# Performance work log

Hardware: AMD Instinct MI355X
Metric: run time of the kernel (lower is better)

## Reference

```python
import jax, jax.numpy as jnp
import numpy as np

B, S, D = 4, 2048, 1024
H, HD = 8, 128
EPS = 1e-5
NEG = -1e30


def layernorm(x, w, b):
    mu = jnp.mean(x, axis=-1, keepdims=True)
    var = jnp.mean(jnp.square(x - mu), axis=-1, keepdims=True)
    return (x - mu) * jax.lax.rsqrt(var + EPS) * w + b


def rmsnorm(x, w):
    ms = jnp.mean(jnp.square(x), axis=-1, keepdims=True)
    return x * jax.lax.rsqrt(ms + EPS) * w


def setup_inputs() -> dict:
    key = jax.random.key(0)
    ks = jax.random.split(key, 8)
    scale = 0.02
    return {
        "layer_input": jax.random.normal(ks[0], (B, S, D), jnp.float32),
        "positions": jnp.broadcast_to(jnp.arange(S, dtype=jnp.int32), (B, S)),
        "ln_in_w": jnp.ones((D,), jnp.float32),
        "ln_in_b": jnp.zeros((D,), jnp.float32),
        "W_uvqk": jax.random.normal(ks[1], (D, 4 * H * HD), jnp.float32) * scale,
        "b_uvqk": jax.random.normal(ks[2], (4 * H * HD,), jnp.float32) * scale,
        "ln_out_w": jnp.ones((H * HD,), jnp.float32),
        "ln_out_b": jnp.zeros((H * HD,), jnp.float32),
        "W_proj": jax.random.normal(ks[3], (H * HD, D), jnp.float32) * scale,
        "rms_w": jnp.ones((D,), jnp.float32),
        "W1": jax.random.normal(ks[4], (D, 2 * D), jnp.float32) * scale,
        "W2": jax.random.normal(ks[5], (D, D), jnp.float32) * scale,
    }


def reference(layer_input, positions, ln_in_w, ln_in_b, W_uvqk, b_uvqk,
              ln_out_w, ln_out_b, W_proj, rms_w, W1, W2):
    # --- HSTU attention block ---
    normed = layernorm(layer_input, ln_in_w, ln_in_b)              # [B,S,D]
    mixed = jax.nn.silu(normed @ W_uvqk + b_uvqk)                  # [B,S,4*H*HD]
    user, value, query, key = jnp.split(mixed, 4, axis=-1)
    q = query.reshape(B, S, H, HD)
    k = key.reshape(B, S, H, HD)
    v = value.reshape(B, S, H, HD)
    alpha = 1.0 / np.sqrt(HD).astype(np.float32)
    scores = jnp.einsum("bqhd,bkhd->bhqk", q, k) * alpha           # [B,H,S,S]
    causal = jnp.tril(jnp.ones((S, S), bool))
    scores = jnp.where(causal, scores, NEG)
    probs = jax.nn.softmax(scores, axis=-1)
    attn = jnp.einsum("bhqk,bkhd->bqhd", probs, v).reshape(B, S, H * HD)
    # output norm * user gate, then projection
    parallel = user * layernorm(attn, ln_out_w, ln_out_b)          # [B,S,H*HD]
    layer_output = parallel @ W_proj                               # [B,S,D]
    # --- residual add + RMSNorm + SwiGLU FFN ---
    summed = layer_output + layer_input
    ffn_in = rmsnorm(summed, rms_w)
    h = ffn_in @ W1                                                # [B,S,2D]
    a, b = jnp.split(h, 2, axis=-1)                                # a <- w3, b <- w1
    ffn_out = (jax.nn.silu(a) * b) @ W2
    return ffn_out + layer_output
```

## Files before the change

### kernel.cpp

```cpp
#include <hip/hip_runtime.h>
#include <stdint.h>

typedef unsigned short u16;
typedef __bf16 bf16x8_t __attribute__((ext_vector_type(8)));
typedef float f32x4_t __attribute__((ext_vector_type(4)));

#define D_MODEL 1024
#define SEQ 2048
#define BATCH 4
#define NROWS (BATCH * SEQ)
#define HDIM 128

constexpr int EPI_UVQK = 0;
constexpr int EPI_F32 = 1;
constexpr int EPI_SILUMUL = 2;
constexpr int EPI_ADD_F32 = 3;

__device__ __forceinline__ float bf2f(u16 u) {
  union { unsigned int i; float f; } v; v.i = ((unsigned int)u) << 16; return v.f;
}
__device__ __forceinline__ u16 f2bf(float f) {
  union { float f; unsigned int i; } v; v.f = f;
  unsigned int r = (v.i + 0x7FFFu + ((v.i >> 16) & 1u)) >> 16;
  return (u16)r;
}
__device__ __forceinline__ float silu_f(float x) { return x / (1.0f + __expf(-x)); }

__device__ __forceinline__ void load_lds16(const void* g, void* l) {
  auto gp = (const __attribute__((address_space(1))) char*)(uintptr_t)g;
  auto lp = (__attribute__((address_space(3))) char*)(uint32_t)(uintptr_t)l;
  __builtin_amdgcn_global_load_lds(gp, lp, 16, 0, 0);
}

__device__ __forceinline__ void block_sum2(float& a, float& b, float* sm) {
  #pragma unroll
  for (int off = 32; off > 0; off >>= 1) {
    a += __shfl_xor(a, off, 64);
    b += __shfl_xor(b, off, 64);
  }
  const int w = threadIdx.x >> 6;
  if ((threadIdx.x & 63) == 0) { sm[w] = a; sm[4 + w] = b; }
  __syncthreads();
  a = sm[0] + sm[1] + sm[2] + sm[3];
  b = sm[4] + sm[5] + sm[6] + sm[7];
}

template <int ILV>
__global__ __launch_bounds__(256)
void k_wconv(const float* __restrict__ W, u16* __restrict__ Wt, int K, int N) {
  __shared__ float tile[32][33];
  const int n0 = blockIdx.x * 32, k0 = blockIdx.y * 32;
  const int tx = threadIdx.x & 31, ty = threadIdx.x >> 5;
  #pragma unroll
  for (int i = 0; i < 4; i++)
    tile[ty + 8 * i][tx] = W[(size_t)(k0 + ty + 8 * i) * N + n0 + tx];
  __syncthreads();
  #pragma unroll
  for (int i = 0; i < 4; i++) {
    const int nlog = n0 + ty + 8 * i;
    int rowp;
    if (ILV == 0) rowp = nlog;
    else rowp = (nlog < 1024) ? (32 * (nlog >> 4) + (nlog & 15))
                              : (32 * ((nlog - 1024) >> 4) + 16 + ((nlog - 1024) & 15));
    Wt[(size_t)rowp * K + k0 + tx] = f2bf(tile[tx][ty + 8 * i]);
  }
}

__global__ __launch_bounds__(256)
void k_ln_in(const float* __restrict__ X, const float* __restrict__ w,
             const float* __restrict__ b, u16* __restrict__ Y) {
  __shared__ float sm[8];
  const int row = blockIdx.x, t = threadIdx.x;
  const float4 v = ((const float4*)(X + (size_t)row * D_MODEL))[t];
  float s = v.x + v.y + v.z + v.w;
  float ss = v.x * v.x + v.y * v.y + v.z * v.z + v.w * v.w;
  block_sum2(s, ss, sm);
  const float mu = s * (1.0f / D_MODEL);
  const float var = ss * (1.0f / D_MODEL) - mu * mu;
  const float rs = rsqrtf(var + 1e-5f);
  const float4 wv = ((const float4*)w)[t];
  const float4 bv = ((const float4*)b)[t];
  ushort4 o;
  o.x = f2bf((v.x - mu) * rs * wv.x + bv.x);
  o.y = f2bf((v.y - mu) * rs * wv.y + bv.y);
  o.z = f2bf((v.z - mu) * rs * wv.z + bv.z);
  o.w = f2bf((v.w - mu) * rs * wv.w + bv.w);
  ((ushort4*)(Y + (size_t)row * D_MODEL))[t] = o;
}

__global__ __launch_bounds__(256)
void k_gated(const u16* __restrict__ attn, const u16* __restrict__ mixed,
             const float* __restrict__ w, const float* __restrict__ b,
             u16* __restrict__ out) {
  __shared__ float sm[8];
  const int row = blockIdx.x, t = threadIdx.x;
  const ushort4 av = ((const ushort4*)(attn + (size_t)row * D_MODEL))[t];
  const float x0 = bf2f(av.x), x1 = bf2f(av.y), x2 = bf2f(av.z), x3 = bf2f(av.w);
  float s = x0 + x1 + x2 + x3;
  float ss = x0 * x0 + x1 * x1 + x2 * x2 + x3 * x3;
  block_sum2(s, ss, sm);
  const float mu = s * (1.0f / D_MODEL);
  const float rs = rsqrtf(ss * (1.0f / D_MODEL) - mu * mu + 1e-5f);
  const ushort4 uv = ((const ushort4*)(mixed + (size_t)row * 4096))[t];
  const float4 wv = ((const float4*)w)[t];
  const float4 bv = ((const float4*)b)[t];
  ushort4 o;
  o.x = f2bf(bf2f(uv.x) * ((x0 - mu) * rs * wv.x + bv.x));
  o.y = f2bf(bf2f(uv.y) * ((x1 - mu) * rs * wv.y + bv.y));
  o.z = f2bf(bf2f(uv.z) * ((x2 - mu) * rs * wv.z + bv.z));
  o.w = f2bf(bf2f(uv.w) * ((x3 - mu) * rs * wv.w + bv.w));
  ((ushort4*)(out + (size_t)row * D_MODEL))[t] = o;
}

__global__ __launch_bounds__(256)
void k_rms(const float* __restrict__ lo, const float* __restrict__ li,
           const float* __restrict__ w, u16* __restrict__ out) {
  __shared__ float sm[8];
  const int row = blockIdx.x, t = threadIdx.x;
  const float4 a = ((const float4*)(lo + (size_t)row * D_MODEL))[t];
  const float4 bq = ((const float4*)(li + (size_t)row * D_MODEL))[t];
  const float x0 = a.x + bq.x, x1 = a.y + bq.y, x2 = a.z + bq.z, x3 = a.w + bq.w;
  float ss = x0 * x0 + x1 * x1 + x2 * x2 + x3 * x3, dummy = 0.f;
  block_sum2(ss, dummy, sm);
  const float rs = rsqrtf(ss * (1.0f / D_MODEL) + 1e-5f);
  const float4 wv = ((const float4*)w)[t];
  ushort4 o;
  o.x = f2bf(x0 * rs * wv.x);
  o.y = f2bf(x1 * rs * wv.y);
  o.z = f2bf(x2 * rs * wv.z);
  o.w = f2bf(x3 * rs * wv.w);
  ((ushort4*)(out + (size_t)row * D_MODEL))[t] = o;
}

template <int EPI>
__global__ __launch_bounds__(256, 2)
void k_gemm(const u16* __restrict__ A, const u16* __restrict__ Bt,
            void* __restrict__ Cout, const float* __restrict__ bias,
            const float* __restrict__ addsrc,
            u16* __restrict__ kc, u16* __restrict__ vtc,
            int M, int N, int K) {
  __shared__ u16 As[128 * 64];
  __shared__ u16 Bs[128 * 64];
  const int t = threadIdx.x, lane = t & 63, w = t >> 6;
  const int l15 = lane & 15, l4 = lane >> 4;
  const int wr = w >> 1, wc = w & 1;
  const int m0 = blockIdx.x * 128, n0 = blockIdx.y * 128;
  const int lr = lane >> 3, lc = lane & 7;
  const int swz = (lc ^ lr) * 8;

  f32x4_t acc[4][4];
  #pragma unroll
  for (int mi = 0; mi < 4; mi++)
    #pragma unroll
    for (int ni = 0; ni < 4; ni++) {
      acc[mi][ni][0] = 0.f; acc[mi][ni][1] = 0.f; acc[mi][ni][2] = 0.f; acc[mi][ni][3] = 0.f;
    }

  const u16* Ab = A + (size_t)m0 * K + swz;
  const u16* Bb = Bt + (size_t)n0 * K + swz;

  for (int kt = 0; kt < K; kt += 64) {
    #pragma unroll
    for (int j = 0; j < 4; j++) {
      const size_t rr = (size_t)((w * 4 + j) * 8 + lr);
      load_lds16(Ab + rr * K + kt, &As[(w * 4 + j) * 512]);
      load_lds16(Bb + rr * K + kt, &Bs[(w * 4 + j) * 512]);
    }
    __syncthreads();
    #pragma unroll
    for (int kk = 0; kk < 2; kk++) {
      bf16x8_t af[4], bf[4];
      #pragma unroll
      for (int mi = 0; mi < 4; mi++) {
        const int row = wr * 64 + mi * 16 + l15;
        const int cph = (kk * 4 + l4) ^ (row & 7);
        af[mi] = *(const bf16x8_t*)&As[row * 64 + cph * 8];
      }
      #pragma unroll
      for (int ni = 0; ni < 4; ni++) {
        const int row = wc * 64 + ni * 16 + l15;
        const int cph = (kk * 4 + l4) ^ (row & 7);
        bf[ni] = *(const bf16x8_t*)&Bs[row * 64 + cph * 8];
      }
      #pragma unroll
      for (int mi = 0; mi < 4; mi++)
        #pragma unroll
        for (int ni = 0; ni < 4; ni++)
          acc[mi][ni] = __builtin_amdgcn_mfma_f32_16x16x32_bf16(af[mi], bf[ni], acc[mi][ni], 0, 0, 0);
    }
    __syncthreads();
  }

  if constexpr (EPI == EPI_SILUMUL) {
    #pragma unroll
    for (int mi = 0; mi < 4; mi++)
      #pragma unroll
      for (int nj = 0; nj < 2; nj++) {
        const int gcol = (n0 >> 1) + wc * 32 + nj * 16 + l15;
        #pragma unroll
        for (int r = 0; r < 4; r++) {
          const size_t row = (size_t)(m0 + wr * 64 + mi * 16 + l4 * 4 + r);
          ((u16*)Cout)[row * 1024 + gcol] =
              f2bf(silu_f(acc[mi][2 * nj][r]) * acc[mi][2 * nj + 1][r]);
        }
      }
  } else {
    #pragma unroll
    for (int mi = 0; mi < 4; mi++) {
      #pragma unroll
      for (int ni = 0; ni < 4; ni++) {
        const int col = n0 + wc * 64 + ni * 16 + l15;
        float bv = 0.f;
        if constexpr (EPI == EPI_UVQK) bv = bias[col];
        if constexpr (EPI == EPI_UVQK) {
          const int rowb = m0 + wr * 64 + mi * 16 + l4 * 4;
          u16 c4[4];
          #pragma unroll
          for (int r = 0; r < 4; r++) c4[r] = f2bf(silu_f(acc[mi][ni][r] + bv));
          if (col < 1024 || (col >= 2048 && col < 3072)) {
            #pragma unroll
            for (int r = 0; r < 4; r++)
              ((u16*)Cout)[(size_t)(rowb + r) * N + col] = c4[r];
          } else if (col < 2048) {
            const int h = (col - 1024) >> 7, d = (col - 1024) & 127;
            const int bI = rowb >> 11, seqr = rowb & 2047;
            const size_t off = ((size_t)(bI * 8 + h) * 32 + (seqr >> 6)) * 8192 + d * 64 + (seqr & 63);
            *(ushort4*)&vtc[off] = *(const ushort4*)c4;
          } else {
            const int h = (col - 3072) >> 7, d = (col - 3072) & 127;
            const int bI = rowb >> 11, seqr = rowb & 2047;
            #pragma unroll
            for (int r = 0; r < 4; r++)
              kc[((size_t)(bI * 8 + h) * 2048 + seqr + r) * 128 + d] = c4[r];
          }
        } else {
          #pragma unroll
          for (int r = 0; r < 4; r++) {
            const size_t row = (size_t)(m0 + wr * 64 + mi * 16 + l4 * 4 + r);
            float v = acc[mi][ni][r];
            if constexpr (EPI == EPI_F32) {
              ((float*)Cout)[row * N + col] = v;
            } else {
              ((float*)Cout)[row * N + col] = v + addsrc[row * N + col];
            }
          }
        }
      }
    }
  }
}

__global__ __launch_bounds__(256, 2)
void k_attn(const u16* __restrict__ mixed, const u16* __restrict__ Kc,
            const u16* __restrict__ Vtc, u16* __restrict__ attnb,
            u16* __restrict__ o_part, float* __restrict__ ml) {
  __shared__ u16 Ks[64 * 128];
  __shared__ u16 Vts[128 * 64];
  __shared__ u16 Ps[4 * 16 * 64];
  const int t = threadIdx.x, lane = t & 63, w = t >> 6;
  const int l15 = lane & 15, l4 = lane >> 4;
  const int f = blockIdx.x;
  const int v = (f & 7) * 96 + (f >> 3);
  const int ci = v % 24, bh = v / 24;
  const int bI = bh >> 3, h = bh & 7;
  int qt, ch;
  if (ci < 16) { qt = 15 - (ci >> 1); ch = ci & 1; }
  else { qt = 23 - ci; ch = 0; }
  const bool split = (qt >= 8);
  const int qb = qt * 128;
  const int nt_all = 2 * qt + 2;
  const int t0 = (split && ch == 1) ? (qt + 1) : 0;
  const int t1 = (split && ch == 0) ? (qt + 1) : nt_all;

  const u16* base = mixed + (size_t)bI * SEQ * 4096;
  const int qcol = 2 * D_MODEL + h * HDIM;
  const int qrow0 = qb + w * 32;
  const u16* Kh = Kc + (size_t)bh * SEQ * 128;
  const u16* Vh = Vtc + (size_t)bh * 32 * 8192;

  const int nk = lane;

  bf16x8_t qf[2][4];
  #pragma unroll
  for (int mi = 0; mi < 2; mi++) {
    const u16* qp = base + (size_t)(qrow0 + mi * 16 + l15) * 4096 + qcol + l4 * 8;
    #pragma unroll
    for (int ks = 0; ks < 4; ks++) qf[mi][ks] = *(const bf16x8_t*)(qp + ks * 32);
  }

  f32x4_t o[2][8];
  #pragma unroll
  for (int mi = 0; mi < 2; mi++)
    #pragma unroll
    for (int df = 0; df < 8; df++) { o[mi][df][0] = 0.f; o[mi][df][1] = 0.f; o[mi][df][2] = 0.f; o[mi][df][3] = 0.f; }
  float mrun[2][4], lrun[2][4];
  #pragma unroll
  for (int mi = 0; mi < 2; mi++)
    #pragma unroll
    for (int r = 0; r < 4; r++) { mrun[mi][r] = -1e30f; lrun[mi][r] = 0.f; }

  const float alpha = 0.08838834764831845f;

  auto stage = [&](int tile) {
    const u16* Kt = Kh + (size_t)(tile * 64) * 128;
    const u16* Vt = Vh + (size_t)tile * 8192;
    #pragma unroll
    for (int j = 0; j < 4; j++) {
      const int slot = j * 4 + w;
      const int kr = slot * 4 + (nk >> 4), gk = nk & 15;
      load_lds16(Kt + kr * 128 + ((gk ^ (kr & 7)) * 8), &Ks[slot * 512]);
      const int d = slot * 8 + (nk >> 3), gv = nk & 7;
      load_lds16(Vt + d * 64 + ((gv ^ (d & 7) ^ ((d >> 3) & 7)) * 8), &Vts[slot * 512]);
    }
  };

  for (int it = t0; it < t1; it++) {
    const int kb = it * 64;
    stage(it);
    __syncthreads();

    const bool active = (kb <= qrow0 + 31);
    const bool needmask = (kb + 63 > qrow0);
    if (active) {
      f32x4_t s[2][4];
      #pragma unroll
      for (int mi = 0; mi < 2; mi++)
        #pragma unroll
        for (int ni = 0; ni < 4; ni++) { s[mi][ni][0] = 0.f; s[mi][ni][1] = 0.f; s[mi][ni][2] = 0.f; s[mi][ni][3] = 0.f; }
      #pragma unroll
      for (int ks = 0; ks < 4; ks++) {
        bf16x8_t kf[4];
        #pragma unroll
        for (int ni = 0; ni < 4; ni++) {
          const int key = ni * 16 + l15;
          const int cph = (ks * 4 + l4) ^ (key & 7);
          kf[ni] = *(const bf16x8_t*)&Ks[key * 128 + cph * 8];
        }
        #pragma unroll
        for (int mi = 0; mi < 2; mi++)
          #pragma unroll
          for (int ni = 0; ni < 4; ni++)
            s[mi][ni] = __builtin_amdgcn_mfma_f32_16x16x32_bf16(qf[mi][ks], kf[ni], s[mi][ni], 0, 0, 0);
      }
      #pragma unroll
      for (int mi = 0; mi < 2; mi++) {
        #pragma unroll
        for (int r = 0; r < 4; r++) {
          const int qr = qrow0 + mi * 16 + l4 * 4 + r;
          float mx = -1e30f;
          #pragma unroll
          for (int ni = 0; ni < 4; ni++) {
            float v2 = s[mi][ni][r] * alpha;
            if (needmask) {
              const int key = kb + ni * 16 + l15;
              if (key > qr) v2 = -1e30f;
            }
            s[mi][ni][r] = v2;
            mx = fmaxf(mx, v2);
          }
          #pragma unroll
          for (int off = 1; off < 16; off <<= 1) mx = fmaxf(mx, __shfl_xor(mx, off, 64));
          const float mnew = fmaxf(mrun[mi][r], mx);
          const float fsc = __expf(mrun[mi][r] - mnew);
          mrun[mi][r] = mnew;
          lrun[mi][r] *= fsc;
          #pragma unroll
          for (int df = 0; df < 8; df++) o[mi][df][r] *= fsc;
          float ls = 0.f;
          #pragma unroll
          for (int ni = 0; ni < 4; ni++) {
            const float p = __expf(s[mi][ni][r] - mnew);
            s[mi][ni][r] = p;
            ls += p;
          }
          #pragma unroll
          for (int off = 1; off < 16; off <<= 1) ls += __shfl_xor(ls, off, 64);
          lrun[mi][r] += ls;
        }
        #pragma unroll
        for (int ni = 0; ni < 4; ni++)
          #pragma unroll
          for (int r = 0; r < 4; r++) {
            const int pr = l4 * 4 + r;
            const int pc = ni * 16 + l15;
            Ps[w * 1024 + pr * 64 + (((pc >> 3) ^ (pr & 7)) * 8) + (pc & 7)] = f2bf(s[mi][ni][r]);
          }
        #pragma unroll
        for (int ks2 = 0; ks2 < 2; ks2++) {
          bf16x8_t pa;
          {
            const int pr = l15;
            const int cph = (ks2 * 4 + l4) ^ (pr & 7);
            pa = *(const bf16x8_t*)&Ps[w * 1024 + pr * 64 + cph * 8];
          }
          #pragma unroll
          for (int df = 0; df < 8; df++) {
            const int d = df * 16 + l15;
            const int cph = (ks2 * 4 + l4) ^ (d & 7) ^ ((d >> 3) & 7);
            const bf16x8_t vb = *(const bf16x8_t*)&Vts[d * 64 + cph * 8];
            o[mi][df] = __builtin_amdgcn_mfma_f32_16x16x32_bf16(pa, vb, o[mi][df], 0, 0, 0);
          }
        }
      }
    }
    __syncthreads();
  }

  if (!split) {
    #pragma unroll
    for (int mi = 0; mi < 2; mi++) {
      #pragma unroll
      for (int r = 0; r < 4; r++) {
        const float inv = 1.0f / lrun[mi][r];
        const size_t row = (size_t)bI * SEQ + qrow0 + mi * 16 + l4 * 4 + r;
        #pragma unroll
        for (int df = 0; df < 8; df++)
          attnb[row * D_MODEL + h * HDIM + df * 16 + l15] = f2bf(o[mi][df][r] * inv);
      }
    }
  } else {
    const int sl = bh * 8 + (qt - 8);
    #pragma unroll
    for (int mi = 0; mi < 2; mi++) {
      #pragma unroll
      for (int r = 0; r < 4; r++) {
        const int pr = w * 32 + mi * 16 + l4 * 4 + r;
        if (l15 == 0) {
          ml[sl * 512 + ch * 256 + pr] = mrun[mi][r];
          ml[sl * 512 + ch * 256 + 128 + pr] = lrun[mi][r];
        }
        if (ch == 0) {
          const size_t row = (size_t)bI * SEQ + qb + pr;
          #pragma unroll
          for (int df = 0; df < 8; df++)
            attnb[row * D_MODEL + h * HDIM + df * 16 + l15] = f2bf(o[mi][df][r]);
        } else {
          #pragma unroll
          for (int df = 0; df < 8; df++)
            o_part[(size_t)sl * 16384 + pr * 128 + df * 16 + l15] = f2bf(o[mi][df][r]);
        }
      }
    }
  }
}

__global__ __launch_bounds__(256)
void k_combine(const u16* __restrict__ o_part, const float* __restrict__ ml,
               u16* __restrict__ attnb) {
  const int qti = blockIdx.x, bh = blockIdx.y;
  const int bI = bh >> 3, h = bh & 7;
  const int t = threadIdx.x;
  const int pr = t >> 1, half = t & 1;
  const int sl = bh * 8 + qti;
  const float m0 = ml[sl * 512 + pr];
  const float l0 = ml[sl * 512 + 128 + pr];
  const float m1 = ml[sl * 512 + 256 + pr];
  const float l1 = ml[sl * 512 + 384 + pr];
  const float M = fmaxf(m0, m1);
  const float w0 = __expf(m0 - M), w1 = __expf(m1 - M);
  const float inv = 1.0f / (w0 * l0 + w1 * l1);
  const float c0 = w0 * inv, c1 = w1 * inv;
  const size_t row = (size_t)bI * SEQ + (8 + qti) * 128 + pr;
  u16* ap = attnb + row * D_MODEL + h * HDIM + half * 64;
  const u16* pp = o_part + (size_t)sl * 16384 + pr * 128 + half * 64;
  #pragma unroll
  for (int j = 0; j < 8; j++) {
    u16 a[8], b[8], c[8];
    *(uint4*)a = ((const uint4*)ap)[j];
    *(uint4*)b = ((const uint4*)pp)[j];
    #pragma unroll
    for (int i = 0; i < 8; i++) c[i] = f2bf(c0 * bf2f(a[i]) + c1 * bf2f(b[i]));
    ((uint4*)ap)[j] = *(const uint4*)c;
  }
}

extern "C" void kernel_launch(void* const* d_in, const int* in_sizes, int n_in,
                              void* d_out, int out_size, void* d_ws, size_t ws_size,
                              hipStream_t stream) {
  (void)in_sizes; (void)n_in; (void)out_size; (void)ws_size;
  const float* layer_input = (const float*)d_in[0];
  const float* ln_in_w  = (const float*)d_in[2];
  const float* ln_in_b  = (const float*)d_in[3];
  const float* W_uvqk   = (const float*)d_in[4];
  const float* b_uvqk   = (const float*)d_in[5];
  const float* ln_out_w = (const float*)d_in[6];
  const float* ln_out_b = (const float*)d_in[7];
  const float* W_proj   = (const float*)d_in[8];
  const float* rms_w    = (const float*)d_in[9];
  const float* W1       = (const float*)d_in[10];
  const float* W2       = (const float*)d_in[11];
  float* out = (float*)d_out;

  char* ws = (char*)d_ws;
  u16* buf0    = (u16*)(ws);
  u16* mixed   = (u16*)(ws + ((size_t)16 << 20));
  u16* attnb   = (u16*)(ws + ((size_t)80 << 20));
  float* lout  = (float*)(ws + ((size_t)96 << 20));
  u16* Kc      = (u16*)(ws + ((size_t)96 << 20));
  u16* Vtc     = (u16*)(ws + ((size_t)112 << 20));
  u16* wt_uvqk = (u16*)(ws + ((size_t)128 << 20));
  u16* wt_proj = (u16*)(ws + ((size_t)136 << 20));
  u16* wt_1    = (u16*)(ws + ((size_t)138 << 20));
  u16* wt_2    = (u16*)(ws + ((size_t)142 << 20));
  u16* o_part  = (u16*)d_out;
  float* ml    = (float*)((char*)d_out + ((size_t)20 << 20));

  k_wconv<0><<<dim3(128, 32), 256, 0, stream>>>(W_uvqk, wt_uvqk, 1024, 4096);
  k_wconv<0><<<dim3(32, 32), 256, 0, stream>>>(W_proj, wt_proj, 1024, 1024);
  k_wconv<1><<<dim3(64, 32), 256, 0, stream>>>(W1, wt_1, 1024, 2048);
  k_wconv<0><<<dim3(32, 32), 256, 0, stream>>>(W2, wt_2, 1024, 1024);

  k_ln_in<<<NROWS, 256, 0, stream>>>(layer_input, ln_in_w, ln_in_b, buf0);
  k_gemm<EPI_UVQK><<<dim3(64, 32), 256, 0, stream>>>(buf0, wt_uvqk, mixed, b_uvqk, nullptr, Kc, Vtc, NROWS, 4096, 1024);
  k_attn<<<768, 256, 0, stream>>>(mixed, Kc, Vtc, attnb, o_part, ml);
  k_combine<<<dim3(8, 32), 256, 0, stream>>>(o_part, ml, attnb);
  k_gated<<<NROWS, 256, 0, stream>>>(attnb, mixed, ln_out_w, ln_out_b, buf0);
  k_gemm<EPI_F32><<<dim3(64, 8), 256, 0, stream>>>(buf0, wt_proj, lout, nullptr, nullptr, nullptr, nullptr, NROWS, 1024, 1024);
  k_rms<<<NROWS, 256, 0, stream>>>(lout, layer_input, rms_w, buf0);
  k_gemm<EPI_SILUMUL><<<dim3(64, 16), 256, 0, stream>>>(buf0, wt_1, mixed, nullptr, nullptr, nullptr, nullptr, NROWS, 2048, 1024);
  k_gemm<EPI_ADD_F32><<<dim3(64, 8), 256, 0, stream>>>(mixed, wt_2, out, nullptr, lout, nullptr, nullptr, NROWS, 1024, 1024);
}
```

Before: 360.6 us.

## Fuse split-KV combine into gated layernorm and store projection output as bf16

```diff
diff --git a/kernel.cpp b/kernel.cpp
--- a/kernel.cpp
+++ b/kernel.cpp
@@ -12,9 +12,9 @@
 #define HDIM 128
 
 constexpr int EPI_UVQK = 0;
-constexpr int EPI_F32 = 1;
+constexpr int EPI_BF16O = 1;
 constexpr int EPI_SILUMUL = 2;
-constexpr int EPI_ADD_F32 = 3;
+constexpr int EPI_ADD_BF16 = 3;
 
 __device__ __forceinline__ float bf2f(u16 u) {
   union { unsigned int i; float f; } v; v.i = ((unsigned int)u) << 16; return v.f;
@@ -91,11 +91,33 @@
 __global__ __launch_bounds__(256)
 void k_gated(const u16* __restrict__ attn, const u16* __restrict__ mixed,
              const float* __restrict__ w, const float* __restrict__ b,
+             const u16* __restrict__ o_part, const float* __restrict__ ml,
              u16* __restrict__ out) {
   __shared__ float sm[8];
   const int row = blockIdx.x, t = threadIdx.x;
+  const int bI = row >> 11, seq = row & 2047;
   const ushort4 av = ((const ushort4*)(attn + (size_t)row * D_MODEL))[t];
-  const float x0 = bf2f(av.x), x1 = bf2f(av.y), x2 = bf2f(av.z), x3 = bf2f(av.w);
+  float x0, x1, x2, x3;
+  if (seq < 1024) {
+    x0 = bf2f(av.x); x1 = bf2f(av.y); x2 = bf2f(av.z); x3 = bf2f(av.w);
+  } else {
+    const int qti = (seq >> 7) - 8, pr = seq & 127;
+    const int h = t >> 5;
+    const int sl = (bI * 8 + h) * 8 + qti;
+    const float m0 = ml[sl * 512 + pr];
+    const float l0 = ml[sl * 512 + 128 + pr];
+    const float m1 = ml[sl * 512 + 256 + pr];
+    const float l1 = ml[sl * 512 + 384 + pr];
+    const float M = fmaxf(m0, m1);
+    const float w0 = __expf(m0 - M), w1 = __expf(m1 - M);
+    const float inv = 1.0f / (w0 * l0 + w1 * l1);
+    const float c0 = w0 * inv, c1 = w1 * inv;
+    const ushort4 bv4 = *(const ushort4*)&o_part[(size_t)sl * 16384 + pr * 128 + ((4 * t) & 127)];
+    x0 = c0 * bf2f(av.x) + c1 * bf2f(bv4.x);
+    x1 = c0 * bf2f(av.y) + c1 * bf2f(bv4.y);
+    x2 = c0 * bf2f(av.z) + c1 * bf2f(bv4.z);
+    x3 = c0 * bf2f(av.w) + c1 * bf2f(bv4.w);
+  }
   float s = x0 + x1 + x2 + x3;
   float ss = x0 * x0 + x1 * x1 + x2 * x2 + x3 * x3;
   block_sum2(s, ss, sm);
@@ -113,13 +135,14 @@
 }
 
 __global__ __launch_bounds__(256)
-void k_rms(const float* __restrict__ lo, const float* __restrict__ li,
+void k_rms(const u16* __restrict__ lo, const float* __restrict__ li,
            const float* __restrict__ w, u16* __restrict__ out) {
   __shared__ float sm[8];
   const int row = blockIdx.x, t = threadIdx.x;
-  const float4 a = ((const float4*)(lo + (size_t)row * D_MODEL))[t];
+  const ushort4 a = ((const ushort4*)(lo + (size_t)row * D_MODEL))[t];
   const float4 bq = ((const float4*)(li + (size_t)row * D_MODEL))[t];
-  const float x0 = a.x + bq.x, x1 = a.y + bq.y, x2 = a.z + bq.z, x3 = a.w + bq.w;
+  const float x0 = bf2f(a.x) + bq.x, x1 = bf2f(a.y) + bq.y;
+  const float x2 = bf2f(a.z) + bq.z, x3 = bf2f(a.w) + bq.w;
   float ss = x0 * x0 + x1 * x1 + x2 * x2 + x3 * x3, dummy = 0.f;
   block_sum2(ss, dummy, sm);
   const float rs = rsqrtf(ss * (1.0f / D_MODEL) + 1e-5f);
@@ -238,10 +261,10 @@
           for (int r = 0; r < 4; r++) {
             const size_t row = (size_t)(m0 + wr * 64 + mi * 16 + l4 * 4 + r);
             float v = acc[mi][ni][r];
-            if constexpr (EPI == EPI_F32) {
-              ((float*)Cout)[row * N + col] = v;
+            if constexpr (EPI == EPI_BF16O) {
+              ((u16*)Cout)[row * N + col] = f2bf(v);
             } else {
-              ((float*)Cout)[row * N + col] = v + addsrc[row * N + col];
+              ((float*)Cout)[row * N + col] = v + bf2f(kc[row * N + col]);
             }
           }
         }
@@ -444,36 +467,6 @@
   }
 }
 
-__global__ __launch_bounds__(256)
-void k_combine(const u16* __restrict__ o_part, const float* __restrict__ ml,
-               u16* __restrict__ attnb) {
-  const int qti = blockIdx.x, bh = blockIdx.y;
-  const int bI = bh >> 3, h = bh & 7;
-  const int t = threadIdx.x;
-  const int pr = t >> 1, half = t & 1;
-  const int sl = bh * 8 + qti;
-  const float m0 = ml[sl * 512 + pr];
-  const float l0 = ml[sl * 512 + 128 + pr];
-  const float m1 = ml[sl * 512 + 256 + pr];
-  const float l1 = ml[sl * 512 + 384 + pr];
-  const float M = fmaxf(m0, m1);
-  const float w0 = __expf(m0 - M), w1 = __expf(m1 - M);
-  const float inv = 1.0f / (w0 * l0 + w1 * l1);
-  const float c0 = w0 * inv, c1 = w1 * inv;
-  const size_t row = (size_t)bI * SEQ + (8 + qti) * 128 + pr;
-  u16* ap = attnb + row * D_MODEL + h * HDIM + half * 64;
-  const u16* pp = o_part + (size_t)sl * 16384 + pr * 128 + half * 64;
-  #pragma unroll
-  for (int j = 0; j < 8; j++) {
-    u16 a[8], b[8], c[8];
-    *(uint4*)a = ((const uint4*)ap)[j];
-    *(uint4*)b = ((const uint4*)pp)[j];
-    #pragma unroll
-    for (int i = 0; i < 8; i++) c[i] = f2bf(c0 * bf2f(a[i]) + c1 * bf2f(b[i]));
-    ((uint4*)ap)[j] = *(const uint4*)c;
-  }
-}
-
 extern "C" void kernel_launch(void* const* d_in, const int* in_sizes, int n_in,
                               void* d_out, int out_size, void* d_ws, size_t ws_size,
                               hipStream_t stream) {
@@ -495,7 +488,7 @@
   u16* buf0    = (u16*)(ws);
   u16* mixed   = (u16*)(ws + ((size_t)16 << 20));
   u16* attnb   = (u16*)(ws + ((size_t)80 << 20));
-  float* lout  = (float*)(ws + ((size_t)96 << 20));
+  u16* lout16  = (u16*)(ws + ((size_t)96 << 20));
   u16* Kc      = (u16*)(ws + ((size_t)96 << 20));
   u16* Vtc     = (u16*)(ws + ((size_t)112 << 20));
   u16* wt_uvqk = (u16*)(ws + ((size_t)128 << 20));
@@ -513,10 +506,9 @@
   k_ln_in<<<NROWS, 256, 0, stream>>>(layer_input, ln_in_w, ln_in_b, buf0);
   k_gemm<EPI_UVQK><<<dim3(64, 32), 256, 0, stream>>>(buf0, wt_uvqk, mixed, b_uvqk, nullptr, Kc, Vtc, NROWS, 4096, 1024);
   k_attn<<<768, 256, 0, stream>>>(mixed, Kc, Vtc, attnb, o_part, ml);
-  k_combine<<<dim3(8, 32), 256, 0, stream>>>(o_part, ml, attnb);
-  k_gated<<<NROWS, 256, 0, stream>>>(attnb, mixed, ln_out_w, ln_out_b, buf0);
-  k_gemm<EPI_F32><<<dim3(64, 8), 256, 0, stream>>>(buf0, wt_proj, lout, nullptr, nullptr, nullptr, nullptr, NROWS, 1024, 1024);
-  k_rms<<<NROWS, 256, 0, stream>>>(lout, layer_input, rms_w, buf0);
+  k_gated<<<NROWS, 256, 0, stream>>>(attnb, mixed, ln_out_w, ln_out_b, o_part, ml, buf0);
+  k_gemm<EPI_BF16O><<<dim3(64, 8), 256, 0, stream>>>(buf0, wt_proj, lout16, nullptr, nullptr, nullptr, nullptr, NROWS, 1024, 1024);
+  k_rms<<<NROWS, 256, 0, stream>>>(lout16, layer_input, rms_w, buf0);
   k_gemm<EPI_SILUMUL><<<dim3(64, 16), 256, 0, stream>>>(buf0, wt_1, mixed, nullptr, nullptr, nullptr, nullptr, NROWS, 2048, 1024);
-  k_gemm<EPI_ADD_F32><<<dim3(64, 8), 256, 0, stream>>>(mixed, wt_2, out, nullptr, lout, nullptr, nullptr, NROWS, 1024, 1024);
-}
+  k_gemm<EPI_ADD_BF16><<<dim3(64, 8), 256, 0, stream>>>(mixed, wt_2, out, nullptr, nullptr, lout16, nullptr, NROWS, 1024, 1024);
+}
```

New measurement: 349.1 us. -3.2%, faster.
